# Kernel optimization log

Hardware: AMD Instinct MI355X
Metric: run time of the kernel (lower is better)

The kernel has to match this reference:

```python
import jax, jax.numpy as jnp
from jax import lax
import numpy as np

BS = 16          # batch (must be even, K % BS == 0)
K = 8192         # MoCo queue size
H = 768          # hidden size
G = 5            # rank_num (number of GMM components)
UPDATE_MEAN = 0.1


def _norm(x):
    return x / jnp.linalg.norm(x, axis=-1, keepdims=True)


def setup_inputs() -> dict:
    key = jax.random.key(0)
    ks = jax.random.split(key, 6)
    sent_q = _norm(jax.random.normal(ks[0], (BS, H), jnp.float32))
    sent_k = _norm(jax.random.normal(ks[1], (BS, H), jnp.float32))
    queue = _norm(jax.random.normal(ks[2], (K, H), jnp.float32))
    mu = jax.random.normal(ks[3], (G, H), jnp.float32)
    lg_sigma2 = jax.random.normal(ks[4], (G, H), jnp.float32)
    pi = jnp.ones((G,), jnp.float32)
    rank_mean = jax.random.uniform(ks[5], (G,), jnp.float32)
    return {"sent_q": sent_q, "sent_k": sent_k, "queue": queue,
            "mu": mu, "lg_sigma2": lg_sigma2, "pi": pi, "rank_mean": rank_mean}


def gaussian_mixture(features, mu, lg_sigma2, pi):
    # features: [B, N, H]; mu/lg_sigma2: [G, H]; pi: [G]
    # expo_{bng} = sum_h (f_{bnh} - mu_{gh})^2 / sigma2_{gh}, expanded so we never
    # materialize the [B, N, G, H] diff tensor the torch code builds.
    inv = jnp.exp(-lg_sigma2)                                   # [G, H]
    expo = (jnp.einsum('bnh,gh->bng', features * features, inv)
            - 2.0 * jnp.einsum('bnh,gh->bng', features, mu * inv)
            + jnp.sum(mu * mu * inv, axis=-1))                  # [B, N, G]
    lg2piD = features.shape[-1] * np.log(2.0 * np.pi).astype(np.float32)
    l_prob = -0.5 * (lg2piD + jnp.sum(lg_sigma2, axis=-1) + expo)
    logits = jax.nn.log_softmax(pi) + l_prob
    logits_norm = logits - jnp.max(logits, axis=-1, keepdims=True)
    prob = jax.nn.softmax(logits_norm, axis=-1)
    return logits_norm, prob


def reference(sent_q, sent_k, queue, mu, lg_sigma2, pi, rank_mean):
    bs = sent_q.shape[0]
    all_feature = jnp.concatenate([sent_k, queue], axis=0)       # [N, H]
    N = all_feature.shape[0]

    # golden mask (is_pair=True): pair j of i is (i + bs//2) mod bs
    pair_label = jnp.concatenate([jnp.arange(bs)[bs // 2:], jnp.arange(bs)[:bs // 2]])
    golden = jnp.arange(bs)[:, None] == pair_label[None, :]      # [bs, bs]
    golden_mask = jnp.concatenate(
        [golden, jnp.zeros((bs, N - bs), bool)], axis=1)         # [bs, N]

    sample_sim = sent_q @ all_feature.T                          # [bs, N]

    # map_scores_to_ranks (rank_mean detached)
    rm = lax.stop_gradient(rank_mean)
    cts_pred = jnp.argmin(jnp.abs(sample_sim[..., None] - rm[None, None, :]), axis=-1)
    cts_dist = jnp.floor((sample_sim + 1.0) / 2.0 * G).astype(jnp.int32)

    # GMM on detached broadcast diff [bs, N, H]
    f = lax.stop_gradient(sent_q)[:, None, :] - lax.stop_gradient(all_feature)[None, :, :]
    gmm_logits, gmm_prob = gaussian_mixture(f, mu, lg_sigma2, pi)
    gmm_pred = jnp.argmax(gmm_prob, axis=-1)                     # [bs, N]

    eye = jnp.arange(bs)[:, None] == jnp.arange(N)[None, :]      # [bs, N]
    # torch: gmm_label aliases cts_pred and is masked_fill_'d in place
    gmm_label = jnp.where(eye | golden_mask, G - 1, cts_pred)

    # update_rank_mean(sample_sim, gmm_pred) -- uses gmm_pred BEFORE cts_label masking
    oh = jax.nn.one_hot(gmm_pred, G, dtype=sample_sim.dtype)     # [bs, N, G]
    counts = jnp.sum(oh, axis=(0, 1))                            # [G]
    sums = jnp.einsum('bng,bn->g', oh, sample_sim)
    cur_rank_mean = sums / (counts + 1e-12)
    upd = (counts != 0).astype(rank_mean.dtype)
    new_rank_mean = (1.0 - upd * UPDATE_MEAN) * rank_mean + upd * UPDATE_MEAN * cur_rank_mean

    # torch: cts_label aliases gmm_pred and masked_fill_ mutates both in place;
    # the returned 'gmm pred' therefore equals this masked version.
    cts_label = jnp.where(golden_mask, G - 1, gmm_pred)

    logits_max = lax.stop_gradient(jnp.max(sample_sim, axis=1, keepdims=True))
    cts_logits = sample_sim - logits_max

    # acc pred: zero the (i, i) entries (torch scatter of 0 at col i)
    acc_pred = sample_sim * (1.0 - eye.astype(sample_sim.dtype))

    return (gmm_logits, gmm_prob, cts_logits, acc_pred, new_rank_mean,
            gmm_label, cts_label, cts_dist)


if __name__ == "__main__":
    outs = reference(**setup_inputs())
    for o in outs:
        print(o.shape, o.dtype)
```

## Files before the change

kernel.cpp:

```cpp
#include <hip/hip_runtime.h>
#include <stdint.h>

#define BS 16
#define KQ 8192
#define NTOT (BS + KQ)
#define H 768
#define G 5
#define UPD 0.1f
#define FPAD 772
#define ROWS 4
#define LG2PID (768.0f * 1.8378770664093453f)

#define SZ_BN   (BS*NTOT)
#define SZ_BNG  (BS*NTOT*G)
#define O_GLOGITS 0
#define O_GPROB   (SZ_BNG)
#define O_CTSLOG  (2*SZ_BNG)
#define O_ACC     (O_CTSLOG + SZ_BN)
#define O_NRM     (O_ACC + SZ_BN)
#define O_GLABEL  (O_NRM + G)
#define O_CLABEL  (O_GLABEL + SZ_BN)
#define O_CDIST   (O_CLABEL + SZ_BN)

#define W_INV   0
#define W_BB    (G*H)
#define W_A2    (W_BB + BS*G)
#define W_CNT8  (W_A2 + NTOT*G)
#define W_SUM8  (W_CNT8 + 128)
#define W_RMX8  (W_SUM8 + 128)
#define W_DIAG  (W_RMX8 + 128)

__device__ __forceinline__ unsigned enc_f(float f) {
    unsigned u = __float_as_uint(f);
    return (u & 0x80000000u) ? ~u : (u | 0x80000000u);
}
__device__ __forceinline__ float dec_f(unsigned k) {
    return (k & 0x80000000u) ? __uint_as_float(k & 0x7fffffffu) : __uint_as_float(~k);
}

__device__ __forceinline__ float wave_red_sum(float v) {
    #pragma unroll
    for (int off = 32; off > 0; off >>= 1) v += __shfl_down(v, off, 64);
    return v;
}

__device__ __forceinline__ void gload_lds16(const float* g, float* l) {
    __builtin_amdgcn_global_load_lds(
        (const __attribute__((address_space(1))) void*)(g),
        (__attribute__((address_space(3))) void*)(l), 16, 0, 0);
}

__global__ __launch_bounds__(256) void k1_kernel(
    const float* __restrict__ sent_q, const float* __restrict__ sent_k,
    const float* __restrict__ queue,  const float* __restrict__ mu,
    const float* __restrict__ lg,     const float* __restrict__ pi,
    float* __restrict__ ws)
{
    const int t = threadIdx.x;
    const int lane = t & 63;
    const int w = t >> 6;
    const int bx = blockIdx.x;

    {
        const int n = bx * ROWS + w;
        const float* f = (n < BS) ? (sent_k + n*H) : (queue + (n - BS) * H);
        float Tp[G] = {0.f,0.f,0.f,0.f,0.f};
        float Vp[G] = {0.f,0.f,0.f,0.f,0.f};
        #pragma unroll
        for (int j = 0; j < 3; ++j) {
            const int h = j*256 + lane*4;
            const float4 fv = *reinterpret_cast<const float4*>(f + h);
            const float fx2 = fv.x*fv.x, fy2 = fv.y*fv.y, fz2 = fv.z*fv.z, fw2 = fv.w*fv.w;
            #pragma unroll
            for (int g = 0; g < G; ++g) {
                const float4 lv = *reinterpret_cast<const float4*>(lg + g*H + h);
                const float4 mv = *reinterpret_cast<const float4*>(mu + g*H + h);
                float ix = expf(-lv.x), iy = expf(-lv.y), iz = expf(-lv.z), iw = expf(-lv.w);
                Tp[g] = fmaf(fx2, ix, Tp[g]);
                Tp[g] = fmaf(fy2, iy, Tp[g]);
                Tp[g] = fmaf(fz2, iz, Tp[g]);
                Tp[g] = fmaf(fw2, iw, Tp[g]);
                Vp[g] = fmaf(fv.x, mv.x*ix, Vp[g]);
                Vp[g] = fmaf(fv.y, mv.y*iy, Vp[g]);
                Vp[g] = fmaf(fv.z, mv.z*iz, Vp[g]);
                Vp[g] = fmaf(fv.w, mv.w*iw, Vp[g]);
            }
        }
        #pragma unroll
        for (int g = 0; g < G; ++g) {
            float T = wave_red_sum(Tp[g]);
            float V = wave_red_sum(Vp[g]);
            if (lane == 0) ws[W_A2 + n*G + g] = 0.5f*T + V;
        }
    }

    if (bx < BS*G) {
        if (w == 0) {
            const int b = bx / G, g = bx % G;
            float accP = 0.f, accU = 0.f, accC = 0.f, accS = 0.f;
            for (int h = lane; h < H; h += 64) {
                float qv  = sent_q[b*H + h];
                float lgv = lg[g*H + h];
                float m   = mu[g*H + h];
                float iv  = expf(-lgv);
                accP = fmaf(qv*qv, iv, accP);
                accU = fmaf(qv*m,  iv, accU);
                accC = fmaf(m*m,   iv, accC);
                accS += lgv;
            }
            accP = wave_red_sum(accP);
            accU = wave_red_sum(accU);
            accC = wave_red_sum(accC);
            accS = wave_red_sum(accS);
            if (lane == 0) {
                float mx = pi[0];
                #pragma unroll
                for (int gg = 1; gg < G; ++gg) mx = fmaxf(mx, pi[gg]);
                float s = 0.f;
                #pragma unroll
                for (int gg = 0; gg < G; ++gg) s += expf(pi[gg] - mx);
                float lse = mx + logf(s);
                ws[W_BB + b*G + g] =
                    (pi[g] - lse) - 0.5f*(LG2PID + accS + accC + accP - 2.f*accU);
            }
        }
    } else if (bx < BS*G + 15) {
        const int i = (bx - BS*G) * 256 + t;
        ws[W_INV + i] = expf(-lg[i]);
    } else if (bx == BS*G + 15) {
        for (int i = t; i < 384; i += 256) ws[W_CNT8 + i] = 0.f;
    }
}

__global__ __launch_bounds__(256, 8) void main_kernel(
    const float* __restrict__ sent_q,
    const float* __restrict__ sent_k,
    const float* __restrict__ queue,
    const float* __restrict__ rank_mean,
    const float* __restrict__ invp,
    const float* __restrict__ BBp,
    const float* __restrict__ A2p,
    float* cnt8, float* sum8, unsigned* rmx8, float* diagp,
    float* __restrict__ out)
{
    __shared__ __align__(16) float fbuf[ROWS * FPAD];
    __shared__ float red[64][21];
    __shared__ float s_BB[BS*G];
    __shared__ float s_A2[ROWS*G];
    __shared__ float s_cnt[G], s_sum[G];

    const int t    = threadIdx.x;
    const int lane = t & 63;
    const int w    = t >> 6;
    const int b    = lane >> 2;
    const int nl   = lane & 3;
    const int bx   = blockIdx.x;
    const int n    = bx * ROWS + nl;

    if (t < BS*G) s_BB[t] = BBp[t];
    if (t >= 128 && t < 128 + ROWS*G) s_A2[t-128] = A2p[bx*ROWS*G + (t-128)];
    if (t >= 160 && t < 160 + G) { s_cnt[t-160] = 0.f; s_sum[t-160] = 0.f; }

    {
        const int rn = bx * ROWS + w;
        const float* src = ((rn < BS) ? (sent_k + rn*H) : (queue + (rn - BS)*H)) + lane*4;
        #pragma unroll
        for (int k = 0; k < 3; ++k)
            gload_lds16(src + k*256, &fbuf[w*FPAD + k*256]);
    }
    __syncthreads();

    const int hu = __builtin_amdgcn_readfirstlane(w * 192);
    const float* qb = sent_q + b*H + hu;
    const float* fb = fbuf + nl*FPAD + hu;
    float sim = 0.f;
    float R[G] = {0.f, 0.f, 0.f, 0.f, 0.f};
    #pragma unroll 4
    for (int i = 0; i < 48; ++i) {
        const float4 qv = *reinterpret_cast<const float4*>(qb + i*4);
        const float4 fv = *reinterpret_cast<const float4*>(fb + i*4);
        float p0 = qv.x * fv.x;
        float p1 = qv.y * fv.y;
        float p2 = qv.z * fv.z;
        float p3 = qv.w * fv.w;
        sim += (p0 + p1) + (p2 + p3);
        #pragma unroll
        for (int g = 0; g < G; ++g) {
            const float* iv = invp + g*H + hu + i*4;
            R[g] = fmaf(p3, iv[3], fmaf(p2, iv[2], fmaf(p1, iv[1], fmaf(p0, iv[0], R[g]))));
        }
    }

    if (w) {
        red[lane][(w-1)*6 + 0] = sim;
        #pragma unroll
        for (int g = 0; g < G; ++g) red[lane][(w-1)*6 + 1 + g] = R[g];
    }
    __syncthreads();

    if (w == 0) {
        #pragma unroll
        for (int qq = 0; qq < 3; ++qq) {
            sim += red[lane][qq*6];
            #pragma unroll
            for (int g = 0; g < G; ++g) R[g] += red[lane][qq*6 + 1 + g];
        }

        float lgt[G];
        #pragma unroll
        for (int g = 0; g < G; ++g)
            lgt[g] = s_BB[b*G + g] - s_A2[nl*G + g] + R[g];
        float mx = lgt[0];
        #pragma unroll
        for (int g = 1; g < G; ++g) mx = fmaxf(mx, lgt[g]);

        const int bn = b * NTOT + n;
        float e[G], se = 0.f;
        #pragma unroll
        for (int g = 0; g < G; ++g) {
            float ln = lgt[g] - mx;
            out[O_GLOGITS + (size_t)bn * G + g] = ln;
            e[g] = expf(ln);
            se += e[g];
        }
        int pred = 0; float bestp = -1.f;
        #pragma unroll
        for (int g = 0; g < G; ++g) {
            float pg = e[g] / se;
            out[O_GPROB + (size_t)bn * G + g] = pg;
            if (pg > bestp) { bestp = pg; pred = g; }
        }

        int cp = 0; float bd = fabsf(sim - rank_mean[0]);
        #pragma unroll
        for (int g = 1; g < G; ++g) {
            float d = fabsf(sim - rank_mean[g]);
            if (d < bd) { bd = d; cp = g; }
        }

        float cdist = floorf((sim + 1.0f) * 0.5f * (float)G);

        bool eyev = (n == b);
        bool gold = (n < BS) && (n == ((b + BS/2) & (BS - 1)));

        out[O_GLABEL + bn] = (eyev || gold) ? (float)(G - 1) : (float)cp;
        out[O_CLABEL + bn] = gold ? (float)(G - 1) : (float)pred;
        out[O_ACC    + bn] = eyev ? 0.f : sim;
        out[O_CDIST  + bn] = cdist;
        if (eyev) diagp[b] = sim;

        atomicAdd(&s_cnt[pred], 1.f);
        atomicAdd(&s_sum[pred], sim);

        float m4 = sim;
        m4 = fmaxf(m4, __shfl_down(m4, 2, 4));
        m4 = fmaxf(m4, __shfl_down(m4, 1, 4));
        if (nl == 0) atomicMax(&rmx8[(bx & 7) * 16 + b], enc_f(m4));
    }
    __syncthreads();
    if (t < G) {
        atomicAdd(&cnt8[(bx & 7) * 16 + t], s_cnt[t]);
        atomicAdd(&sum8[(bx & 7) * 16 + t], s_sum[t]);
    }
}

__global__ __launch_bounds__(256) void final_kernel(
    const float* __restrict__ rank_mean,
    const float* __restrict__ cnt8, const float* __restrict__ sum8,
    const unsigned* __restrict__ rmx8, const float* __restrict__ diagp,
    float* __restrict__ out)
{
    const int i4 = blockIdx.x * 256 + threadIdx.x;
    if (i4 < G) {
        float c = 0.f, s = 0.f;
        #pragma unroll
        for (int j = 0; j < 8; ++j) { c += cnt8[j*16 + i4]; s += sum8[j*16 + i4]; }
        float cur = s / (c + 1e-12f);
        float u = (c != 0.f) ? 1.f : 0.f;
        out[O_NRM + i4] = (1.f - u * UPD) * rank_mean[i4] + u * UPD * cur;
    }
    if (i4 >= SZ_BN/4) return;
    const int i0 = i4 * 4;
    const int b  = i0 / NTOT;
    const int n0 = i0 - b * NTOT;
    unsigned mk = 0u;
    #pragma unroll
    for (int j = 0; j < 8; ++j) mk = max(mk, rmx8[j*16 + b]);
    const float rm = dec_f(mk);
    float4 v = *reinterpret_cast<const float4*>(&out[O_ACC + i0]);
    if (b >= n0 && b < n0 + 4) {
        float d = diagp[b];
        int r = b - n0;
        if (r == 0) v.x = d; else if (r == 1) v.y = d;
        else if (r == 2) v.z = d; else v.w = d;
    }
    float4 o;
    o.x = v.x - rm; o.y = v.y - rm; o.z = v.z - rm; o.w = v.w - rm;
    *reinterpret_cast<float4*>(&out[O_CTSLOG + i0]) = o;
}

extern "C" void kernel_launch(void* const* d_in, const int* in_sizes, int n_in,
                              void* d_out, int out_size, void* d_ws, size_t ws_size,
                              hipStream_t stream) {
    const float* sent_q    = (const float*)d_in[0];
    const float* sent_k    = (const float*)d_in[1];
    const float* queue     = (const float*)d_in[2];
    const float* mu        = (const float*)d_in[3];
    const float* lg        = (const float*)d_in[4];
    const float* pi        = (const float*)d_in[5];
    const float* rank_mean = (const float*)d_in[6];
    float* out = (float*)d_out;
    float* ws  = (float*)d_ws;

    k1_kernel<<<NTOT / ROWS, 256, 0, stream>>>(
        sent_q, sent_k, queue, mu, lg, pi, ws);

    main_kernel<<<NTOT / ROWS, 256, 0, stream>>>(
        sent_q, sent_k, queue, rank_mean,
        ws + W_INV, ws + W_BB, ws + W_A2,
        ws + W_CNT8, ws + W_SUM8,
        reinterpret_cast<unsigned*>(ws + W_RMX8), ws + W_DIAG,
        out);

    final_kernel<<<(SZ_BN/4 + 255) / 256, 256, 0, stream>>>(
        rank_mean, ws + W_CNT8, ws + W_SUM8,
        reinterpret_cast<const unsigned*>(ws + W_RMX8), ws + W_DIAG,
        out);
}
```

Before: 135.9 us.

## Fuse per-row GMM A2 computation into main kernel, shrink prep kernel

The per-row quadratic terms (sum f^2*inv and f*mu*inv) move out of the first kernel and into the main kernel, where they use the feature rows already staged in LDS and the precomputed inv from the workspace. The first kernel now only computes the batch-by-component constants, the inv table and the counter zeroing, using 36 blocks instead of one per row group. This avoids reading the whole queue twice from global memory and removes the A2 round-trip through the workspace. The cost is extra work and register pressure in the main kernel, which is launched with an occupancy bound.

```diff
diff --git a/kernel.cpp b/kernel.cpp
--- a/kernel.cpp
+++ b/kernel.cpp
@@ -24,8 +24,7 @@
 
 #define W_INV   0
 #define W_BB    (G*H)
-#define W_A2    (W_BB + BS*G)
-#define W_CNT8  (W_A2 + NTOT*G)
+#define W_CNT8  (W_BB + BS*G)
 #define W_SUM8  (W_CNT8 + 128)
 #define W_RMX8  (W_SUM8 + 128)
 #define W_DIAG  (W_RMX8 + 128)
@@ -50,9 +49,8 @@
         (__attribute__((address_space(3))) void*)(l), 16, 0, 0);
 }
 
-__global__ __launch_bounds__(256) void k1_kernel(
-    const float* __restrict__ sent_q, const float* __restrict__ sent_k,
-    const float* __restrict__ queue,  const float* __restrict__ mu,
+__global__ __launch_bounds__(256) void prep_kernel(
+    const float* __restrict__ sent_q, const float* __restrict__ mu,
     const float* __restrict__ lg,     const float* __restrict__ pi,
     float* __restrict__ ws)
 {
@@ -61,73 +59,39 @@
     const int w = t >> 6;
     const int bx = blockIdx.x;
 
-    {
-        const int n = bx * ROWS + w;
-        const float* f = (n < BS) ? (sent_k + n*H) : (queue + (n - BS) * H);
-        float Tp[G] = {0.f,0.f,0.f,0.f,0.f};
-        float Vp[G] = {0.f,0.f,0.f,0.f,0.f};
-        #pragma unroll
-        for (int j = 0; j < 3; ++j) {
-            const int h = j*256 + lane*4;
-            const float4 fv = *reinterpret_cast<const float4*>(f + h);
-            const float fx2 = fv.x*fv.x, fy2 = fv.y*fv.y, fz2 = fv.z*fv.z, fw2 = fv.w*fv.w;
+    if (bx < 20) {
+        const int task = bx * 4 + w;
+        const int b = task / G, g = task % G;
+        float accP = 0.f, accU = 0.f, accC = 0.f, accS = 0.f;
+        for (int h = lane; h < H; h += 64) {
+            float qv  = sent_q[b*H + h];
+            float lgv = lg[g*H + h];
+            float m   = mu[g*H + h];
+            float iv  = expf(-lgv);
+            accP = fmaf(qv*qv, iv, accP);
+            accU = fmaf(qv*m,  iv, accU);
+            accC = fmaf(m*m,   iv, accC);
+            accS += lgv;
+        }
+        accP = wave_red_sum(accP);
+        accU = wave_red_sum(accU);
+        accC = wave_red_sum(accC);
+        accS = wave_red_sum(accS);
+        if (lane == 0) {
+            float mx = pi[0];
             #pragma unroll
-            for (int g = 0; g < G; ++g) {
-                const float4 lv = *reinterpret_cast<const float4*>(lg + g*H + h);
-                const float4 mv = *reinterpret_cast<const float4*>(mu + g*H + h);
-                float ix = expf(-lv.x), iy = expf(-lv.y), iz = expf(-lv.z), iw = expf(-lv.w);
-                Tp[g] = fmaf(fx2, ix, Tp[g]);
-                Tp[g] = fmaf(fy2, iy, Tp[g]);
-                Tp[g] = fmaf(fz2, iz, Tp[g]);
-                Tp[g] = fmaf(fw2, iw, Tp[g]);
-                Vp[g] = fmaf(fv.x, mv.x*ix, Vp[g]);
-                Vp[g] = fmaf(fv.y, mv.y*iy, Vp[g]);
-                Vp[g] = fmaf(fv.z, mv.z*iz, Vp[g]);
-                Vp[g] = fmaf(fv.w, mv.w*iw, Vp[g]);
-            }
-        }
-        #pragma unroll
-        for (int g = 0; g < G; ++g) {
-            float T = wave_red_sum(Tp[g]);
-            float V = wave_red_sum(Vp[g]);
-            if (lane == 0) ws[W_A2 + n*G + g] = 0.5f*T + V;
-        }
-    }
-
-    if (bx < BS*G) {
-        if (w == 0) {
-            const int b = bx / G, g = bx % G;
-            float accP = 0.f, accU = 0.f, accC = 0.f, accS = 0.f;
-            for (int h = lane; h < H; h += 64) {
-                float qv  = sent_q[b*H + h];
-                float lgv = lg[g*H + h];
-                float m   = mu[g*H + h];
-                float iv  = expf(-lgv);
-                accP = fmaf(qv*qv, iv, accP);
-                accU = fmaf(qv*m,  iv, accU);
-                accC = fmaf(m*m,   iv, accC);
-                accS += lgv;
-            }
-            accP = wave_red_sum(accP);
-            accU = wave_red_sum(accU);
-            accC = wave_red_sum(accC);
-            accS = wave_red_sum(accS);
-            if (lane == 0) {
-                float mx = pi[0];
-                #pragma unroll
-                for (int gg = 1; gg < G; ++gg) mx = fmaxf(mx, pi[gg]);
-                float s = 0.f;
-                #pragma unroll
-                for (int gg = 0; gg < G; ++gg) s += expf(pi[gg] - mx);
-                float lse = mx + logf(s);
-                ws[W_BB + b*G + g] =
-                    (pi[g] - lse) - 0.5f*(LG2PID + accS + accC + accP - 2.f*accU);
-            }
-        }
-    } else if (bx < BS*G + 15) {
-        const int i = (bx - BS*G) * 256 + t;
+            for (int gg = 1; gg < G; ++gg) mx = fmaxf(mx, pi[gg]);
+            float s = 0.f;
+            #pragma unroll
+            for (int gg = 0; gg < G; ++gg) s += expf(pi[gg] - mx);
+            float lse = mx + logf(s);
+            ws[W_BB + task] =
+                (pi[g] - lse) - 0.5f*(LG2PID + accS + accC + accP - 2.f*accU);
+        }
+    } else if (bx < 35) {
+        const int i = (bx - 20) * 256 + t;
         ws[W_INV + i] = expf(-lg[i]);
-    } else if (bx == BS*G + 15) {
+    } else {
         for (int i = t; i < 384; i += 256) ws[W_CNT8 + i] = 0.f;
     }
 }
@@ -138,8 +102,8 @@
     const float* __restrict__ queue,
     const float* __restrict__ rank_mean,
     const float* __restrict__ invp,
+    const float* __restrict__ mup,
     const float* __restrict__ BBp,
-    const float* __restrict__ A2p,
     float* cnt8, float* sum8, unsigned* rmx8, float* diagp,
     float* __restrict__ out)
 {
@@ -158,7 +122,6 @@
     const int n    = bx * ROWS + nl;
 
     if (t < BS*G) s_BB[t] = BBp[t];
-    if (t >= 128 && t < 128 + ROWS*G) s_A2[t-128] = A2p[bx*ROWS*G + (t-128)];
     if (t >= 160 && t < 160 + G) { s_cnt[t-160] = 0.f; s_sum[t-160] = 0.f; }
 
     {
@@ -169,6 +132,37 @@
             gload_lds16(src + k*256, &fbuf[w*FPAD + k*256]);
     }
     __syncthreads();
+
+    {
+        const float* frow = fbuf + w*FPAD;
+        float Tp[G] = {0.f,0.f,0.f,0.f,0.f};
+        float Vp[G] = {0.f,0.f,0.f,0.f,0.f};
+        #pragma unroll
+        for (int j = 0; j < 3; ++j) {
+            const int h = j*256 + lane*4;
+            const float4 fv = *reinterpret_cast<const float4*>(frow + h);
+            const float fx2 = fv.x*fv.x, fy2 = fv.y*fv.y, fz2 = fv.z*fv.z, fw2 = fv.w*fv.w;
+            #pragma unroll
+            for (int g = 0; g < G; ++g) {
+                const float4 iv = *reinterpret_cast<const float4*>(invp + g*H + h);
+                const float4 mv = *reinterpret_cast<const float4*>(mup + g*H + h);
+                Tp[g] = fmaf(fx2, iv.x, Tp[g]);
+                Tp[g] = fmaf(fy2, iv.y, Tp[g]);
+                Tp[g] = fmaf(fz2, iv.z, Tp[g]);
+                Tp[g] = fmaf(fw2, iv.w, Tp[g]);
+                Vp[g] = fmaf(fv.x, mv.x*iv.x, Vp[g]);
+                Vp[g] = fmaf(fv.y, mv.y*iv.y, Vp[g]);
+                Vp[g] = fmaf(fv.z, mv.z*iv.z, Vp[g]);
+                Vp[g] = fmaf(fv.w, mv.w*iv.w, Vp[g]);
+            }
+        }
+        #pragma unroll
+        for (int g = 0; g < G; ++g) {
+            float T = wave_red_sum(Tp[g]);
+            float V = wave_red_sum(Vp[g]);
+            if (lane == 0) s_A2[w*G + g] = 0.5f*T + V;
+        }
+    }
 
     const int hu = __builtin_amdgcn_readfirstlane(w * 192);
     const float* qb = sent_q + b*H + hu;
@@ -312,12 +306,11 @@
     float* out = (float*)d_out;
     float* ws  = (float*)d_ws;
 
-    k1_kernel<<<NTOT / ROWS, 256, 0, stream>>>(
-        sent_q, sent_k, queue, mu, lg, pi, ws);
+    prep_kernel<<<36, 256, 0, stream>>>(sent_q, mu, lg, pi, ws);
 
     main_kernel<<<NTOT / ROWS, 256, 0, stream>>>(
         sent_q, sent_k, queue, rank_mean,
-        ws + W_INV, ws + W_BB, ws + W_A2,
+        ws + W_INV, mu, ws + W_BB,
         ws + W_CNT8, ws + W_SUM8,
         reinterpret_cast<unsigned*>(ws + W_RMX8), ws + W_DIAG,
         out);
```

Measured after the change: 208.1 us. 1.53x slower.
